# Optimization experiments

Measured on AMD Instinct MI355X. Metric: run time of the kernel, lower is better.

Reference implementation:

```python
import jax, jax.numpy as jnp
import numpy as np

N, E = 100000, 500000
IN_CH, OUT_CH, MSG_DIM, TIME_DIM, HEADS = 128, 128, 128, 128, 2
C = OUT_CH // HEADS  # per-head channels
EDGE_DIM = MSG_DIM + TIME_DIM


def setup_inputs() -> dict:
    key = jax.random.key(0)
    ks = jax.random.split(key, 16)
    inp = {
        "x": jax.random.normal(ks[0], (N, IN_CH), jnp.float32),
        "last_update": jax.random.uniform(ks[1], (N,), jnp.float32) * 1000.0,
        "t": jax.random.uniform(ks[2], (E,), jnp.float32) * 1000.0,
        "msg": jax.random.normal(ks[3], (E, MSG_DIM), jnp.float32),
        "edge_index": jax.random.randint(ks[4], (2, E), 0, N, jnp.int64),
        # TimeEncoder: Linear(1, TIME_DIM) then cos
        "time_w": jax.random.normal(ks[5], (TIME_DIM,), jnp.float32) / jnp.sqrt(1.0),
        "time_b": jax.random.normal(ks[6], (TIME_DIM,), jnp.float32) * 0.02,
        # TransformerConv linears (stored [in, out] for x @ W)
        "Wq": jax.random.normal(ks[7], (IN_CH, HEADS * C), jnp.float32) / np.sqrt(IN_CH),
        "bq": jnp.zeros((HEADS * C,), jnp.float32),
        "Wk": jax.random.normal(ks[8], (IN_CH, HEADS * C), jnp.float32) / np.sqrt(IN_CH),
        "bk": jnp.zeros((HEADS * C,), jnp.float32),
        "Wv": jax.random.normal(ks[9], (IN_CH, HEADS * C), jnp.float32) / np.sqrt(IN_CH),
        "bv": jnp.zeros((HEADS * C,), jnp.float32),
        "We": jax.random.normal(ks[10], (EDGE_DIM, HEADS * C), jnp.float32) / np.sqrt(EDGE_DIM),  # lin_edge, no bias
        "Wskip": jax.random.normal(ks[11], (IN_CH, HEADS * C), jnp.float32) / np.sqrt(IN_CH),
        "bskip": jnp.zeros((HEADS * C,), jnp.float32),
    }
    return inp


def reference(x, last_update, t, msg, edge_index, time_w, time_b,
              Wq, bq, Wk, bk, Wv, bv, We, Wskip, bskip):
    src = edge_index[0]
    dst = edge_index[1]

    # relative time encoding: cos(Linear(1 -> TIME_DIM))
    rel_t = t - last_update[src]                              # [E]
    rel_t_enc = jnp.cos(rel_t[:, None] * time_w[None, :] + time_b[None, :])  # [E, T]
    edge_attr = jnp.concatenate([rel_t_enc, msg], axis=-1)    # [E, EDGE_DIM]

    # project nodes, then gather per-edge (query at dst, key/value at src)
    q = (x @ Wq + bq).reshape(N, HEADS, C)[dst]               # [E, H, C]
    k = (x @ Wk + bk).reshape(N, HEADS, C)[src]
    v = (x @ Wv + bv).reshape(N, HEADS, C)[src]
    e = (edge_attr @ We).reshape(E, HEADS, C)                 # [E, H, C]

    k = k + e
    alpha = jnp.sum(q * k, axis=-1) / jnp.sqrt(jnp.float32(C))  # [E, H]

    # segment softmax over edges sharing the same destination node
    m = jax.ops.segment_max(alpha, dst, num_segments=N)       # [N, H]
    alpha = jnp.exp(alpha - m[dst])
    s = jax.ops.segment_sum(alpha, dst, num_segments=N)       # [N, H]
    alpha = alpha / (s[dst] + 1e-16)

    # weighted value (value also receives edge projection), scatter-add to dst
    out_e = (v + e) * alpha[..., None]                        # [E, H, C]
    out = jax.ops.segment_sum(out_e, dst, num_segments=N)     # [N, H, C]
    out = out.reshape(N, HEADS * C)

    # root/skip connection
    out = out + x @ Wskip + bskip
    return out
```

## Files before the change

kernel.cpp:

```cpp
#include <hip/hip_runtime.h>
#include <hip/hip_bf16.h>

#define NN 100000
#define EE 500000

typedef __attribute__((ext_vector_type(8))) short short8v;
typedef __attribute__((ext_vector_type(4))) float f32x4;

__device__ __forceinline__ short f2bf(float f) {
  unsigned u = __builtin_bit_cast(unsigned, f);
  u += 0x7fffu + ((u >> 16) & 1u);
  return (short)(u >> 16);
}

__device__ __forceinline__ void barlds() {
  asm volatile("s_waitcnt lgkmcnt(0)" ::: "memory");
  __builtin_amdgcn_s_barrier();
  asm volatile("" ::: "memory");
}

__global__ __launch_bounds__(256) void k_prep(
    const float* __restrict__ Wq, const float* __restrict__ Wk,
    const float* __restrict__ Wv, const float* __restrict__ Wsk,
    const float* __restrict__ We,
    short* __restrict__ Btfrag, short* __restrict__ Wefrag)
{
  int idx = blockIdx.x * 256 + threadIdx.x;
  if (idx < 65536) {
    int b = idx & 7, lane = (idx >> 3) & 63, kt = (idx >> 9) & 3, tn = (idx >> 11) & 7, cb = idx >> 14;
    int k = kt * 32 + (lane >> 4) * 8 + b;
    int c = tn * 16 + (lane & 15);
    const float* W = cb == 0 ? Wq : cb == 1 ? Wk : cb == 2 ? Wv : Wsk;
    Btfrag[idx] = f2bf(W[k * 128 + c]);
  } else if (idx < 98304) {
    int i2 = idx - 65536;
    int b = i2 & 7, lane = (i2 >> 3) & 63, kt = (i2 >> 9) & 7, strip = i2 >> 12;
    int k = kt * 32 + (lane >> 4) * 8 + b;
    int c = strip * 16 + (lane & 15);
    Wefrag[i2] = f2bf(We[k * 128 + c]);
  }
}

__global__ __launch_bounds__(256) void k_xcast(const float* __restrict__ x,
                                               unsigned short* __restrict__ xb)
{
  size_t base = ((size_t)blockIdx.x * 256 + threadIdx.x) * 8;
  f32x4 a = *(const f32x4*)(x + base);
  f32x4 b = *(const f32x4*)(x + base + 4);
  short8v w;
  #pragma unroll
  for (int j = 0; j < 4; ++j) { w[j] = f2bf(a[j]); w[4 + j] = f2bf(b[j]); }
  *(short8v*)(xb + base) = w;
}

__global__ __launch_bounds__(256) void k_zero(int* __restrict__ p, int n)
{
  int i = blockIdx.x * 256 + threadIdx.x;
  if (i < n) p[i] = 0;
}

__global__ __launch_bounds__(256) void k_hist(const int* __restrict__ ei, int* __restrict__ cnt)
{
  int e = blockIdx.x * 256 + threadIdx.x;
  if (e < EE) atomicAdd(&cnt[ei[EE + e]], 1);
}

__global__ __launch_bounds__(256) void k_scan_a(const int* __restrict__ cnt,
    int* __restrict__ offtmp, int* __restrict__ bsum)
{
  __shared__ int sc[256];
  int t = threadIdx.x;
  int i = blockIdx.x * 256 + t;
  int v = (i < NN) ? cnt[i] : 0;
  sc[t] = v;
  __syncthreads();
  for (int d = 1; d < 256; d <<= 1) {
    int add = (t >= d) ? sc[t - d] : 0;
    __syncthreads();
    sc[t] += add;
    __syncthreads();
  }
  if (i < NN) offtmp[i] = sc[t] - v;
  if (t == 255) bsum[blockIdx.x] = sc[255];
}

__global__ __launch_bounds__(512) void k_scan_b(const int* __restrict__ bsum,
                                                int* __restrict__ bbase)
{
  __shared__ int sc[512];
  int t = threadIdx.x;
  int v = (t < 391) ? bsum[t] : 0;
  sc[t] = v;
  __syncthreads();
  for (int d = 1; d < 512; d <<= 1) {
    int add = (t >= d) ? sc[t - d] : 0;
    __syncthreads();
    sc[t] += add;
    __syncthreads();
  }
  bbase[t] = sc[t] - v;
}

__global__ __launch_bounds__(256) void k_scatter(const int* __restrict__ ei,
    const int* __restrict__ offtmp, const int* __restrict__ bbase,
    int* __restrict__ cur, int* __restrict__ sorted)
{
  int e = blockIdx.x * 256 + threadIdx.x;
  if (e < EE) {
    int d = ei[EE + e];
    int pos = offtmp[d] + bbase[d >> 8] + atomicAdd(&cur[d], 1);
    sorted[pos] = e;
  }
}

__global__ __launch_bounds__(256) void k_emeta(const int* __restrict__ ei,
    const float* __restrict__ tt, const float* __restrict__ lu,
    const int* __restrict__ sorted, int4* __restrict__ emeta)
{
  int i = blockIdx.x * 256 + threadIdx.x;
  if (i < EE) {
    int eid = sorted[i];
    int sv = ei[eid];
    int4 m;
    m.x = eid; m.y = sv; m.z = ei[EE + eid];
    m.w = __float_as_int(tt[eid] - lu[sv]);
    emeta[i] = m;
  }
}

__global__ __launch_bounds__(512) void k_mperm(const float* __restrict__ msg,
    const int* __restrict__ sorted, unsigned short* __restrict__ msgp)
{
  int t = blockIdx.x * 512 + threadIdx.x;
  int i = t >> 4;
  int c = t & 15;
  if (i < EE) {
    int eid = sorted[i];
    const float* mp = msg + (size_t)eid * 128 + c * 8;
    f32x4 m0 = *(const f32x4*)mp, m1 = *(const f32x4*)(mp + 4);
    short8v w;
    #pragma unroll
    for (int j = 0; j < 4; ++j) { w[j] = f2bf(m0[j]); w[4 + j] = f2bf(m1[j]); }
    *(short8v*)(msgp + (size_t)i * 128 + c * 8) = w;
  }
}

template<int USE_MP>
__global__ __launch_bounds__(512) void k_main(
    const unsigned short* __restrict__ xb, const float* __restrict__ msg,
    const unsigned short* __restrict__ msgp,
    const float* __restrict__ tw, const float* __restrict__ tb,
    const short* __restrict__ Btfrag, const short* __restrict__ Wefrag,
    const float* __restrict__ bq, const float* __restrict__ bk,
    const float* __restrict__ bv, const float* __restrict__ bsk,
    const int* __restrict__ offtmp, const int* __restrict__ bbase,
    const int4* __restrict__ emeta, float* __restrict__ out)
{
  __shared__ short R[24576];
  __shared__ short QL[64 * 128];
  __shared__ float sdenL[128];
  __shared__ int dslot[64];

  short* const XS = R;
  short* const EAT = R + 8192;
  short* const KL = R;
  short* const VT = R + 8192;
  short* const PLm = R + 16384;
  short* const PLm2 = R + 20480;

  const int tid = threadIdx.x;
  const int nb0 = blockIdx.x * 64;
  const int wid = tid >> 6, lane = tid & 63;
  const int g = lane >> 4, lr = lane & 15, l7 = lr & 7;
  const int el = tid >> 3, p = tid & 7;
  const int er7 = el & 7;
  const int psw = p ^ er7;
  const int cme = wid * 16 + lr;
  const int cmeh = cme >> 3, cml = cme & 7;

  const float bqc = bq[cme], bkc = bk[cme], bvc = bv[cme], bskc = bsk[cme];
  const short8v ONEB = {16256,16256,16256,16256,16256,16256,16256,16256};

  {
    int node = nb0 + el;
    short8v a = {0,0,0,0,0,0,0,0}, b = a;
    if (node < NN) {
      const unsigned short* xp = xb + (size_t)node * 128 + p * 8;
      a = *(const short8v*)xp;
      b = *(const short8v*)(xp + 64);
    }
    *(short8v*)&XS[el * 128 + psw * 8] = a;
    *(short8v*)&XS[el * 128 + psw * 8 + 64] = b;
  }
  barlds();
  {
    f32x4 qacc[4], skacc[4];
    #pragma unroll
    for (int eg = 0; eg < 4; ++eg) {
      qacc[eg] = (f32x4){0.f, 0.f, 0.f, 0.f};
      skacc[eg] = qacc[eg];
    }
    #pragma unroll
    for (int kt = 0; kt < 4; ++kt) {
      short8v bqf = *(const short8v*)(Btfrag + (size_t)(((0 + wid) * 4 + kt) * 64 + lane) * 8);
      short8v bsf = *(const short8v*)(Btfrag + (size_t)(((24 + wid) * 4 + kt) * 64 + lane) * 8);
      const int sw = (((kt << 2) | g) ^ l7) << 3;
      #pragma unroll
      for (int eg = 0; eg < 4; ++eg) {
        const short8v a = *(const short8v*)&XS[(eg * 16 + lr) * 128 + sw];
        qacc[eg] = __builtin_amdgcn_mfma_f32_16x16x32_bf16(a, bqf, qacc[eg], 0, 0, 0);
        skacc[eg] = __builtin_amdgcn_mfma_f32_16x16x32_bf16(a, bsf, skacc[eg], 0, 0, 0);
      }
    }
    #pragma unroll
    for (int eg = 0; eg < 4; ++eg)
      #pragma unroll
      for (int rg = 0; rg < 4; ++rg) {
        int row = eg * 16 + g * 4 + rg;
        int node = nb0 + row;
        QL[row * 128 + ((cmeh ^ (row & 7)) << 3) + cml] = f2bf(qacc[eg][rg] + bqc);
        if (node < NN) out[(size_t)node * 128 + cme] = skacc[eg][rg] + bskc;
      }
  }

  const int beg = offtmp[nb0] + bbase[nb0 >> 8];
  const int end = (nb0 + 64 < NN) ? (offtmp[nb0 + 64] + bbase[(nb0 + 64) >> 8]) : EE;

  f32x4 acc[4], sdacc;
  #pragma unroll
  for (int rtt = 0; rtt < 4; ++rtt) acc[rtt] = (f32x4){0.f, 0.f, 0.f, 0.f};
  sdacc = (f32x4){0.f, 0.f, 0.f, 0.f};

  int pdst = 0; float prelt = 0.f; bool pval = false;
  short8v px0 = {0,0,0,0,0,0,0,0}, px1 = px0, pmb0 = px0, pmb1 = px0;
  {
    int i = beg + el;
    pval = i < end;
    if (pval) {
      int4 m = emeta[i];
      pdst = m.z; prelt = __int_as_float(m.w);
      const unsigned short* xp = xb + (size_t)m.y * 128 + p * 8;
      px0 = *(const short8v*)xp;
      px1 = *(const short8v*)(xp + 64);
      if constexpr (USE_MP) {
        const unsigned short* mp = msgp + (size_t)i * 128 + p * 8;
        pmb0 = *(const short8v*)mp;
        pmb1 = *(const short8v*)(mp + 64);
      } else {
        const float* mp = msg + (size_t)m.x * 128 + p * 8;
        f32x4 m0 = *(const f32x4*)mp,        m1 = *(const f32x4*)(mp + 4);
        f32x4 m2 = *(const f32x4*)(mp + 64), m3 = *(const f32x4*)(mp + 68);
        #pragma unroll
        for (int j = 0; j < 4; ++j) {
          pmb0[j] = f2bf(m0[j]); pmb0[4 + j] = f2bf(m1[j]);
          pmb1[j] = f2bf(m2[j]); pmb1[4 + j] = f2bf(m3[j]);
        }
      }
    }
  }
  barlds();

  for (int t0 = beg; t0 < end; t0 += 64) {
    if (p == 0) dslot[el] = pval ? (pdst - nb0) : -1;
    *(short8v*)&XS[el * 128 + psw * 8] = px0;
    *(short8v*)&XS[el * 128 + psw * 8 + 64] = px1;
    *(short8v*)&EAT[el * 256 + 128 + psw * 8] = pmb0;
    *(short8v*)&EAT[el * 256 + 128 + psw * 8 + 64] = pmb1;
    {
      f32x4 w0 = *(const f32x4*)(tw + p * 8),      w1 = *(const f32x4*)(tw + p * 8 + 4);
      f32x4 b0 = *(const f32x4*)(tb + p * 8),      b1 = *(const f32x4*)(tb + p * 8 + 4);
      f32x4 w2 = *(const f32x4*)(tw + p * 8 + 64), w3 = *(const f32x4*)(tw + p * 8 + 68);
      f32x4 b2 = *(const f32x4*)(tb + p * 8 + 64), b3 = *(const f32x4*)(tb + p * 8 + 68);
      short8v ta, tb2;
      #pragma unroll
      for (int j = 0; j < 4; ++j) {
        ta[j]      = f2bf(__cosf(fmaf(prelt, w0[j], b0[j])));
        ta[4 + j]  = f2bf(__cosf(fmaf(prelt, w1[j], b1[j])));
        tb2[j]     = f2bf(__cosf(fmaf(prelt, w2[j], b2[j])));
        tb2[4 + j] = f2bf(__cosf(fmaf(prelt, w3[j], b3[j])));
      }
      *(short8v*)&EAT[el * 256 + psw * 8] = ta;
      *(short8v*)&EAT[el * 256 + psw * 8 + 64] = tb2;
    }
    barlds();

    {
      int i = t0 + 64 + el;
      pval = i < end;
      if (pval) {
        int4 m = emeta[i];
        pdst = m.z; prelt = __int_as_float(m.w);
        const unsigned short* xp = xb + (size_t)m.y * 128 + p * 8;
        px0 = *(const short8v*)xp;
        px1 = *(const short8v*)(xp + 64);
        if constexpr (USE_MP) {
          const unsigned short* mp = msgp + (size_t)i * 128 + p * 8;
          pmb0 = *(const short8v*)mp;
          pmb1 = *(const short8v*)(mp + 64);
        } else {
          const float* mp = msg + (size_t)m.x * 128 + p * 8;
          f32x4 m0 = *(const f32x4*)mp,        m1 = *(const f32x4*)(mp + 4);
          f32x4 m2 = *(const f32x4*)(mp + 64), m3 = *(const f32x4*)(mp + 68);
          #pragma unroll
          for (int j = 0; j < 4; ++j) {
            pmb0[j] = f2bf(m0[j]); pmb0[4 + j] = f2bf(m1[j]);
            pmb1[j] = f2bf(m2[j]); pmb1[4 + j] = f2bf(m3[j]);
          }
        }
      }
    }

    f32x4 ae[4];
    ae[0] = (f32x4){0.f, 0.f, 0.f, 0.f}; ae[1] = ae[0]; ae[2] = ae[0]; ae[3] = ae[0];
    #pragma unroll
    for (int kt = 0; kt < 8; ++kt) {
      short8v wef = *(const short8v*)(Wefrag + (size_t)((wid * 8 + kt) * 64 + lane) * 8);
      const int sw = (((kt << 2) | g) ^ l7) << 3;
      #pragma unroll
      for (int eg = 0; eg < 4; ++eg) {
        const short8v a = *(const short8v*)&EAT[(eg * 16 + lr) * 256 + sw];
        ae[eg] = __builtin_amdgcn_mfma_f32_16x16x32_bf16(a, wef, ae[eg], 0, 0, 0);
      }
    }
    f32x4 ak[4], av[4];
    ak[0] = (f32x4){0.f, 0.f, 0.f, 0.f}; ak[1] = ak[0]; ak[2] = ak[0]; ak[3] = ak[0];
    av[0] = ak[0]; av[1] = ak[0]; av[2] = ak[0]; av[3] = ak[0];
    #pragma unroll
    for (int kt = 0; kt < 4; ++kt) {
      short8v wkf = *(const short8v*)(Btfrag + (size_t)(((8 + wid) * 4 + kt) * 64 + lane) * 8);
      short8v wvf = *(const short8v*)(Btfrag + (size_t)(((16 + wid) * 4 + kt) * 64 + lane) * 8);
      const int sw = (((kt << 2) | g) ^ l7) << 3;
      #pragma unroll
      for (int eg = 0; eg < 4; ++eg) {
        const short8v a = *(const short8v*)&XS[(eg * 16 + lr) * 128 + sw];
        ak[eg] = __builtin_amdgcn_mfma_f32_16x16x32_bf16(a, wkf, ak[eg], 0, 0, 0);
        av[eg] = __builtin_amdgcn_mfma_f32_16x16x32_bf16(a, wvf, av[eg], 0, 0, 0);
      }
    }
    barlds();

    #pragma unroll
    for (int eg = 0; eg < 4; ++eg)
      #pragma unroll
      for (int rg = 0; rg < 4; ++rg) {
        int e = eg * 16 + g * 4 + rg;
        float kh = ak[eg][rg] + bkc + ae[eg][rg];
        float vh = av[eg][rg] + bvc + ae[eg][rg];
        KL[e * 128 + ((cmeh ^ (e & 7)) << 3) + cml] = f2bf(kh);
        VT[cme * 64 + ((((e >> 3) ^ cml)) << 3) + (e & 7)] = f2bf(vh);
      }
    barlds();

    {
      const int rt = wid >> 1, ct0 = (wid & 1) * 2;
      short8v qa[4];
      #pragma unroll
      for (int kt = 0; kt < 4; ++kt)
        qa[kt] = *(const short8v*)&QL[(rt * 16 + lr) * 128 + ((((kt << 2) | g) ^ l7) << 3)];
      #pragma unroll
      for (int c2 = 0; c2 < 2; ++c2) {
        const int ct = ct0 + c2;
        f32x4 s0 = (f32x4){0.f, 0.f, 0.f, 0.f};
        f32x4 s1 = (f32x4){0.f, 0.f, 0.f, 0.f};
        #pragma unroll
        for (int kt = 0; kt < 4; ++kt) {
          const short8v kbf = *(const short8v*)&KL[(ct * 16 + lr) * 128 + ((((kt << 2) | g) ^ l7) << 3)];
          if (kt < 2) s0 = __builtin_amdgcn_mfma_f32_16x16x32_bf16(qa[kt], kbf, s0, 0, 0, 0);
          else        s1 = __builtin_amdgcn_mfma_f32_16x16x32_bf16(qa[kt], kbf, s1, 0, 0, 0);
        }
        const int col = ct * 16 + lr;
        const int dsc = dslot[col];
        #pragma unroll
        for (int rg = 0; rg < 4; ++rg) {
          int row = rt * 16 + g * 4 + rg;
          bool hit = (dsc == row);
          float pv0 = hit ? __expf(s0[rg] * 0.125f) : 0.f;
          float pv1 = hit ? __expf(s1[rg] * 0.125f) : 0.f;
          int off = row * 64 + ((((col >> 3) ^ (row & 7))) << 3) + (col & 7);
          PLm[off] = f2bf(pv0);
          PLm2[off] = f2bf(pv1);
        }
      }
    }
    barlds();

    {
      const short* PH = (wid < 4) ? PLm : PLm2;
      const int rt4 = wid & 3;
      const short8v vb0 = *(const short8v*)&VT[cme * 64 + ((g ^ cml) << 3)];
      const short8v vb1 = *(const short8v*)&VT[cme * 64 + (((4 | g) ^ cml) << 3)];
      #pragma unroll
      for (int rtt = 0; rtt < 4; ++rtt) {
        const short8v pa0 = *(const short8v*)&PH[(rtt * 16 + lr) * 64 + ((g ^ l7) << 3)];
        const short8v pa1 = *(const short8v*)&PH[(rtt * 16 + lr) * 64 + (((4 | g) ^ l7) << 3)];
        acc[rtt] = __builtin_amdgcn_mfma_f32_16x16x32_bf16(pa0, vb0, acc[rtt], 0, 0, 0);
        acc[rtt] = __builtin_amdgcn_mfma_f32_16x16x32_bf16(pa1, vb1, acc[rtt], 0, 0, 0);
        if (rt4 == rtt) {
          sdacc = __builtin_amdgcn_mfma_f32_16x16x32_bf16(pa0, ONEB, sdacc, 0, 0, 0);
          sdacc = __builtin_amdgcn_mfma_f32_16x16x32_bf16(pa1, ONEB, sdacc, 0, 0, 0);
        }
      }
    }
    barlds();
  }

  if (lr == 0) {
    #pragma unroll
    for (int rg = 0; rg < 4; ++rg)
      sdenL[(wid >> 2) * 64 + (wid & 3) * 16 + g * 4 + rg] = sdacc[rg];
  }
  barlds();
  #pragma unroll
  for (int rtt = 0; rtt < 4; ++rtt)
    #pragma unroll
    for (int rg = 0; rg < 4; ++rg) {
      int row = rtt * 16 + g * 4 + rg;
      int node = nb0 + row;
      if (node < NN) {
        float den = sdenL[(wid >> 2) * 64 + row] + 1e-16f;
        size_t o = (size_t)node * 128 + cme;
        out[o] = out[o] + acc[rtt][rg] / den;
      }
    }
}

extern "C" void kernel_launch(void* const* d_in, const int* in_sizes, int n_in,
                              void* d_out, int out_size, void* d_ws, size_t ws_size,
                              hipStream_t stream) {
  const float* x    = (const float*)d_in[0];
  const float* lu   = (const float*)d_in[1];
  const float* tt   = (const float*)d_in[2];
  const float* msg  = (const float*)d_in[3];
  const int*   ei   = (const int*)d_in[4];
  const float* timew = (const float*)d_in[5];
  const float* timeb = (const float*)d_in[6];
  const float* Wq   = (const float*)d_in[7];
  const float* bq   = (const float*)d_in[8];
  const float* Wk   = (const float*)d_in[9];
  const float* bk   = (const float*)d_in[10];
  const float* Wv   = (const float*)d_in[11];
  const float* bv   = (const float*)d_in[12];
  const float* We   = (const float*)d_in[13];
  const float* Wsk  = (const float*)d_in[14];
  const float* bsk  = (const float*)d_in[15];
  float* out = (float*)d_out;

  char* wsp = (char*)d_ws;
  unsigned short* xbw  = (unsigned short*)wsp;
  short* Btfrag = (short*)(wsp + 51200000);
  short* Wefrag = (short*)(wsp + 51331072);
  int* cnt      = (int*)(wsp + 51404800);
  int* cur      = (int*)(wsp + 51804800);
  int* offtmp   = (int*)(wsp + 52204800);
  int* bsum     = (int*)(wsp + 52605184);
  int* bbase    = (int*)(wsp + 52607232);
  int* sorted   = (int*)(wsp + 52609280);
  int4* emeta   = (int4*)(wsp + 54609280);
  unsigned short* msgp = (unsigned short*)(wsp + 62609280);
  const int use_mp = (ws_size >= (size_t)190609280) ? 1 : 0;

  k_zero<<<782, 256, 0, stream>>>(cnt, 200000);
  k_prep<<<384, 256, 0, stream>>>(Wq, Wk, Wv, Wsk, We, Btfrag, Wefrag);
  k_xcast<<<6250, 256, 0, stream>>>(x, xbw);
  k_hist<<<1954, 256, 0, stream>>>(ei, cnt);
  k_scan_a<<<391, 256, 0, stream>>>(cnt, offtmp, bsum);
  k_scan_b<<<1, 512, 0, stream>>>(bsum, bbase);
  k_scatter<<<1954, 256, 0, stream>>>(ei, offtmp, bbase, cur, sorted);
  k_emeta<<<1954, 256, 0, stream>>>(ei, tt, lu, sorted, emeta);
  if (use_mp) {
    k_mperm<<<15625, 512, 0, stream>>>(msg, sorted, msgp);
    k_main<1><<<1563, 512, 0, stream>>>(xbw, msg, msgp, timew, timeb,
                                        Btfrag, Wefrag, bq, bk, bv, bsk,
                                        offtmp, bbase, emeta, out);
  } else {
    k_main<0><<<1563, 512, 0, stream>>>(xbw, msg, msgp, timew, timeb,
                                        Btfrag, Wefrag, bq, bk, bv, bsk,
                                        offtmp, bbase, emeta, out);
  }
}
```

Measured before the change: 465.9 us.

## Un-alias LDS buffers, hoist weight fragments to registers, pack VT stores

Gives each LDS buffer its own storage instead of aliasing XS/EAT with KL/VT/PLm, which lets two barriers be dropped. The We/Wk/Wv MFMA fragments are loaded into registers once per block instead of inside the loops. VT is written as packed 4-element vectors using a new XOR swizzle, replacing scalar 2-byte stores. LDS use grows to roughly 100KB and register pressure rises, which may cut occupancy.

```diff
diff --git a/kernel.cpp b/kernel.cpp
--- a/kernel.cpp
+++ b/kernel.cpp
@@ -5,6 +5,7 @@
 #define EE 500000
 
 typedef __attribute__((ext_vector_type(8))) short short8v;
+typedef __attribute__((ext_vector_type(4))) short short4v;
 typedef __attribute__((ext_vector_type(4))) float f32x4;
 
 __device__ __forceinline__ short f2bf(float f) {
@@ -156,17 +157,15 @@
     const int* __restrict__ offtmp, const int* __restrict__ bbase,
     const int4* __restrict__ emeta, float* __restrict__ out)
 {
-  __shared__ short R[24576];
+  __shared__ short XS[64 * 128];
+  __shared__ short EAT[64 * 256];
+  __shared__ short KL[64 * 128];
+  __shared__ short VT[128 * 64];
+  __shared__ short PLm[64 * 64];
+  __shared__ short PLm2[64 * 64];
   __shared__ short QL[64 * 128];
   __shared__ float sdenL[128];
   __shared__ int dslot[64];
-
-  short* const XS = R;
-  short* const EAT = R + 8192;
-  short* const KL = R;
-  short* const VT = R + 8192;
-  short* const PLm = R + 16384;
-  short* const PLm2 = R + 20480;
 
   const int tid = threadIdx.x;
   const int nb0 = blockIdx.x * 64;
@@ -177,9 +176,20 @@
   const int psw = p ^ er7;
   const int cme = wid * 16 + lr;
   const int cmeh = cme >> 3, cml = cme & 7;
+  const int s2e = cme & 14;
 
   const float bqc = bq[cme], bkc = bk[cme], bvc = bv[cme], bskc = bsk[cme];
   const short8v ONEB = {16256,16256,16256,16256,16256,16256,16256,16256};
+
+  short8v wef[8], wkf[4], wvf[4];
+  #pragma unroll
+  for (int kt = 0; kt < 8; ++kt)
+    wef[kt] = *(const short8v*)(Wefrag + (size_t)((wid * 8 + kt) * 64 + lane) * 8);
+  #pragma unroll
+  for (int kt = 0; kt < 4; ++kt) {
+    wkf[kt] = *(const short8v*)(Btfrag + (size_t)(((8 + wid) * 4 + kt) * 64 + lane) * 8);
+    wvf[kt] = *(const short8v*)(Btfrag + (size_t)(((16 + wid) * 4 + kt) * 64 + lane) * 8);
+  }
 
   {
     int node = nb0 + el;
@@ -314,12 +324,11 @@
     ae[0] = (f32x4){0.f, 0.f, 0.f, 0.f}; ae[1] = ae[0]; ae[2] = ae[0]; ae[3] = ae[0];
     #pragma unroll
     for (int kt = 0; kt < 8; ++kt) {
-      short8v wef = *(const short8v*)(Wefrag + (size_t)((wid * 8 + kt) * 64 + lane) * 8);
       const int sw = (((kt << 2) | g) ^ l7) << 3;
       #pragma unroll
       for (int eg = 0; eg < 4; ++eg) {
         const short8v a = *(const short8v*)&EAT[(eg * 16 + lr) * 256 + sw];
-        ae[eg] = __builtin_amdgcn_mfma_f32_16x16x32_bf16(a, wef, ae[eg], 0, 0, 0);
+        ae[eg] = __builtin_amdgcn_mfma_f32_16x16x32_bf16(a, wef[kt], ae[eg], 0, 0, 0);
       }
     }
     f32x4 ak[4], av[4];
@@ -327,28 +336,27 @@
     av[0] = ak[0]; av[1] = ak[0]; av[2] = ak[0]; av[3] = ak[0];
     #pragma unroll
     for (int kt = 0; kt < 4; ++kt) {
-      short8v wkf = *(const short8v*)(Btfrag + (size_t)(((8 + wid) * 4 + kt) * 64 + lane) * 8);
-      short8v wvf = *(const short8v*)(Btfrag + (size_t)(((16 + wid) * 4 + kt) * 64 + lane) * 8);
       const int sw = (((kt << 2) | g) ^ l7) << 3;
       #pragma unroll
       for (int eg = 0; eg < 4; ++eg) {
         const short8v a = *(const short8v*)&XS[(eg * 16 + lr) * 128 + sw];
-        ak[eg] = __builtin_amdgcn_mfma_f32_16x16x32_bf16(a, wkf, ak[eg], 0, 0, 0);
-        av[eg] = __builtin_amdgcn_mfma_f32_16x16x32_bf16(a, wvf, av[eg], 0, 0, 0);
-      }
-    }
-    barlds();
-
-    #pragma unroll
-    for (int eg = 0; eg < 4; ++eg)
+        ak[eg] = __builtin_amdgcn_mfma_f32_16x16x32_bf16(a, wkf[kt], ak[eg], 0, 0, 0);
+        av[eg] = __builtin_amdgcn_mfma_f32_16x16x32_bf16(a, wvf[kt], av[eg], 0, 0, 0);
+      }
+    }
+    #pragma unroll
+    for (int eg = 0; eg < 4; ++eg) {
+      short4v vpack;
       #pragma unroll
       for (int rg = 0; rg < 4; ++rg) {
         int e = eg * 16 + g * 4 + rg;
         float kh = ak[eg][rg] + bkc + ae[eg][rg];
         float vh = av[eg][rg] + bvc + ae[eg][rg];
         KL[e * 128 + ((cmeh ^ (e & 7)) << 3) + cml] = f2bf(kh);
-        VT[cme * 64 + ((((e >> 3) ^ cml)) << 3) + (e & 7)] = f2bf(vh);
-      }
+        vpack[rg] = f2bf(vh);
+      }
+      *(short4v*)&VT[cme * 64 + ((((eg << 2) | g) ^ s2e) << 2)] = vpack;
+    }
     barlds();
 
     {
@@ -387,8 +395,8 @@
     {
       const short* PH = (wid < 4) ? PLm : PLm2;
       const int rt4 = wid & 3;
-      const short8v vb0 = *(const short8v*)&VT[cme * 64 + ((g ^ cml) << 3)];
-      const short8v vb1 = *(const short8v*)&VT[cme * 64 + (((4 | g) ^ cml) << 3)];
+      const short8v vb0 = *(const short8v*)&VT[cme * 64 + (((2 * g) ^ s2e) << 2)];
+      const short8v vb1 = *(const short8v*)&VT[cme * 64 + (((2 * (4 | g)) ^ s2e) << 2)];
       #pragma unroll
       for (int rtt = 0; rtt < 4; ++rtt) {
         const short8v pa0 = *(const short8v*)&PH[(rtt * 16 + lr) * 64 + ((g ^ l7) << 3)];
@@ -401,9 +409,9 @@
         }
       }
     }
-    barlds();
-  }
-
+  }
+
+  barlds();
   if (lr == 0) {
     #pragma unroll
     for (int rg = 0; rg < 4; ++rg)
```

Result: slower. 498.3 us (+7.0%).

## Fuse edge metadata into scatter, cast msg unpermuted, keep skip in registers

Applied to the files above, without the earlier changes.

The scatter kernel now writes the per-edge metadata (edge id, source, dest, relative time) straight to its sorted position, which removes the separate sorted-index array and the k_emeta pass. The message tensor is cast to bf16 in its original order with the existing cast kernel instead of being permuted by sorted index. The main kernel then gathers msg rows by edge id, making that read random instead of sequential. The skip projection stays in registers and is added in the final output write, which removes one write and one read-modify-write of the output.

```diff
diff --git a/kernel.cpp b/kernel.cpp
--- a/kernel.cpp
+++ b/kernel.cpp
@@ -102,53 +102,26 @@
 }
 
 __global__ __launch_bounds__(256) void k_scatter(const int* __restrict__ ei,
+    const float* __restrict__ tt, const float* __restrict__ lu,
     const int* __restrict__ offtmp, const int* __restrict__ bbase,
-    int* __restrict__ cur, int* __restrict__ sorted)
+    int* __restrict__ cur, int4* __restrict__ emeta)
 {
   int e = blockIdx.x * 256 + threadIdx.x;
   if (e < EE) {
     int d = ei[EE + e];
     int pos = offtmp[d] + bbase[d >> 8] + atomicAdd(&cur[d], 1);
-    sorted[pos] = e;
-  }
-}
-
-__global__ __launch_bounds__(256) void k_emeta(const int* __restrict__ ei,
-    const float* __restrict__ tt, const float* __restrict__ lu,
-    const int* __restrict__ sorted, int4* __restrict__ emeta)
-{
-  int i = blockIdx.x * 256 + threadIdx.x;
-  if (i < EE) {
-    int eid = sorted[i];
-    int sv = ei[eid];
+    int sv = ei[e];
     int4 m;
-    m.x = eid; m.y = sv; m.z = ei[EE + eid];
-    m.w = __float_as_int(tt[eid] - lu[sv]);
-    emeta[i] = m;
-  }
-}
-
-__global__ __launch_bounds__(512) void k_mperm(const float* __restrict__ msg,
-    const int* __restrict__ sorted, unsigned short* __restrict__ msgp)
-{
-  int t = blockIdx.x * 512 + threadIdx.x;
-  int i = t >> 4;
-  int c = t & 15;
-  if (i < EE) {
-    int eid = sorted[i];
-    const float* mp = msg + (size_t)eid * 128 + c * 8;
-    f32x4 m0 = *(const f32x4*)mp, m1 = *(const f32x4*)(mp + 4);
-    short8v w;
-    #pragma unroll
-    for (int j = 0; j < 4; ++j) { w[j] = f2bf(m0[j]); w[4 + j] = f2bf(m1[j]); }
-    *(short8v*)(msgp + (size_t)i * 128 + c * 8) = w;
+    m.x = e; m.y = sv; m.z = d;
+    m.w = __float_as_int(tt[e] - lu[sv]);
+    emeta[pos] = m;
   }
 }
 
 template<int USE_MP>
 __global__ __launch_bounds__(512) void k_main(
     const unsigned short* __restrict__ xb, const float* __restrict__ msg,
-    const unsigned short* __restrict__ msgp,
+    const unsigned short* __restrict__ msgb,
     const float* __restrict__ tw, const float* __restrict__ tb,
     const short* __restrict__ Btfrag, const short* __restrict__ Wefrag,
     const float* __restrict__ bq, const float* __restrict__ bk,
@@ -193,12 +166,13 @@
     *(short8v*)&XS[el * 128 + psw * 8 + 64] = b;
   }
   barlds();
+  f32x4 skp[4];
   {
-    f32x4 qacc[4], skacc[4];
+    f32x4 qacc[4];
     #pragma unroll
     for (int eg = 0; eg < 4; ++eg) {
       qacc[eg] = (f32x4){0.f, 0.f, 0.f, 0.f};
-      skacc[eg] = qacc[eg];
+      skp[eg] = qacc[eg];
     }
     #pragma unroll
     for (int kt = 0; kt < 4; ++kt) {
@@ -209,7 +183,7 @@
       for (int eg = 0; eg < 4; ++eg) {
         const short8v a = *(const short8v*)&XS[(eg * 16 + lr) * 128 + sw];
         qacc[eg] = __builtin_amdgcn_mfma_f32_16x16x32_bf16(a, bqf, qacc[eg], 0, 0, 0);
-        skacc[eg] = __builtin_amdgcn_mfma_f32_16x16x32_bf16(a, bsf, skacc[eg], 0, 0, 0);
+        skp[eg] = __builtin_amdgcn_mfma_f32_16x16x32_bf16(a, bsf, skp[eg], 0, 0, 0);
       }
     }
     #pragma unroll
@@ -217,9 +191,7 @@
       #pragma unroll
       for (int rg = 0; rg < 4; ++rg) {
         int row = eg * 16 + g * 4 + rg;
-        int node = nb0 + row;
         QL[row * 128 + ((cmeh ^ (row & 7)) << 3) + cml] = f2bf(qacc[eg][rg] + bqc);
-        if (node < NN) out[(size_t)node * 128 + cme] = skacc[eg][rg] + bskc;
       }
   }
 
@@ -243,7 +215,7 @@
       px0 = *(const short8v*)xp;
       px1 = *(const short8v*)(xp + 64);
       if constexpr (USE_MP) {
-        const unsigned short* mp = msgp + (size_t)i * 128 + p * 8;
+        const unsigned short* mp = msgb + (size_t)m.x * 128 + p * 8;
         pmb0 = *(const short8v*)mp;
         pmb1 = *(const short8v*)(mp + 64);
       } else {
@@ -294,7 +266,7 @@
         px0 = *(const short8v*)xp;
         px1 = *(const short8v*)(xp + 64);
         if constexpr (USE_MP) {
-          const unsigned short* mp = msgp + (size_t)i * 128 + p * 8;
+          const unsigned short* mp = msgb + (size_t)m.x * 128 + p * 8;
           pmb0 = *(const short8v*)mp;
           pmb1 = *(const short8v*)(mp + 64);
         } else {
@@ -418,8 +390,7 @@
       int node = nb0 + row;
       if (node < NN) {
         float den = sdenL[(wid >> 2) * 64 + row] + 1e-16f;
-        size_t o = (size_t)node * 128 + cme;
-        out[o] = out[o] + acc[rtt][rg] / den;
+        out[(size_t)node * 128 + cme] = skp[rtt][rg] + bskc + acc[rtt][rg] / den;
       }
     }
 }
@@ -454,26 +425,24 @@
   int* offtmp   = (int*)(wsp + 52204800);
   int* bsum     = (int*)(wsp + 52605184);
   int* bbase    = (int*)(wsp + 52607232);
-  int* sorted   = (int*)(wsp + 52609280);
   int4* emeta   = (int4*)(wsp + 54609280);
-  unsigned short* msgp = (unsigned short*)(wsp + 62609280);
+  unsigned short* msgb = (unsigned short*)(wsp + 62609280);
   const int use_mp = (ws_size >= (size_t)190609280) ? 1 : 0;
 
   k_zero<<<782, 256, 0, stream>>>(cnt, 200000);
   k_prep<<<384, 256, 0, stream>>>(Wq, Wk, Wv, Wsk, We, Btfrag, Wefrag);
   k_xcast<<<6250, 256, 0, stream>>>(x, xbw);
+  if (use_mp) k_xcast<<<31250, 256, 0, stream>>>(msg, msgb);
   k_hist<<<1954, 256, 0, stream>>>(ei, cnt);
   k_scan_a<<<391, 256, 0, stream>>>(cnt, offtmp, bsum);
   k_scan_b<<<1, 512, 0, stream>>>(bsum, bbase);
-  k_scatter<<<1954, 256, 0, stream>>>(ei, offtmp, bbase, cur, sorted);
-  k_emeta<<<1954, 256, 0, stream>>>(ei, tt, lu, sorted, emeta);
+  k_scatter<<<1954, 256, 0, stream>>>(ei, tt, lu, offtmp, bbase, cur, emeta);
   if (use_mp) {
-    k_mperm<<<15625, 512, 0, stream>>>(msg, sorted, msgp);
-    k_main<1><<<1563, 512, 0, stream>>>(xbw, msg, msgp, timew, timeb,
+    k_main<1><<<1563, 512, 0, stream>>>(xbw, msg, msgb, timew, timeb,
                                         Btfrag, Wefrag, bq, bk, bv, bsk,
                                         offtmp, bbase, emeta, out);
   } else {
-    k_main<0><<<1563, 512, 0, stream>>>(xbw, msg, msgp, timew, timeb,
+    k_main<0><<<1563, 512, 0, stream>>>(xbw, msg, msgb, timew, timeb,
                                         Btfrag, Wefrag, bq, bk, bv, bsk,
                                         offtmp, bbase, emeta, out);
   }
```

After: 418.4 us (median of 2 runs). -10.2%, faster.
